# Optimization experiments

Hardware: AMD Instinct MI355X
Metric: run time of the kernel (lower is better)

## Reference

```python
import jax, jax.numpy as jnp
import numpy as np

B, N, D = 4, 2048, 1024
H = 16
DH = D // H


def setup_inputs() -> dict:
    key = jax.random.key(0)
    ks = jax.random.split(key, 9)
    s_in = 1.0 / np.sqrt(D)
    x = jax.random.normal(ks[0], (B, N, D), dtype=jnp.float32)
    Wq = jax.random.uniform(ks[1], (D, D), jnp.float32, -s_in, s_in)
    bq = jax.random.uniform(ks[2], (D,), jnp.float32, -s_in, s_in)
    Wk = jax.random.uniform(ks[3], (D, D), jnp.float32, -s_in, s_in)
    bk = jax.random.uniform(ks[4], (D,), jnp.float32, -s_in, s_in)
    Wv = jax.random.uniform(ks[5], (D, D), jnp.float32, -s_in, s_in)
    bv = jax.random.uniform(ks[6], (D,), jnp.float32, -s_in, s_in)
    Wo = jax.random.uniform(ks[7], (D, D), jnp.float32, -s_in, s_in)
    bo = jax.random.uniform(ks[8], (D,), jnp.float32, -s_in, s_in)
    return {"x": x, "Wq": Wq, "bq": bq, "Wk": Wk, "bk": bk,
            "Wv": Wv, "bv": bv, "Wo": Wo, "bo": bo}


def reference(x, Wq, bq, Wk, bk, Wv, bv, Wo, bo):
    b, n, d = x.shape
    q = (x @ Wq + bq).reshape(b, n, H, DH)  # (b, n, h, dh)
    k = (x @ Wk + bk).reshape(b, n, H, DH)
    v = (x @ Wv + bv).reshape(b, n, H, DH)
    scale = 1.0 / jnp.sqrt(jnp.asarray(DH, x.dtype))
    scores = jnp.einsum("bqhd,bkhd->bhqk", q, k) * scale  # (b, h, n, n)
    # valid = arange(1..n) per query => causal mask: key index < valid[q] = q+1
    causal = jnp.arange(n)[None, :] <= jnp.arange(n)[:, None]  # (n_q, n_k)
    scores = jnp.where(causal[None, None, :, :], scores, -jnp.inf)
    weights = jax.nn.softmax(scores, axis=-1)
    out = jnp.einsum("bhqk,bkhd->bqhd", weights, v).reshape(b, n, d)
    return out @ Wo + bo
```

## Files before the change

### kernel.cpp

```cpp
#include <hip/hip_runtime.h>
#include <hip/hip_bf16.h>
#include <math.h>

namespace {
constexpr int B_ = 4, N_ = 2048, D_ = 1024, H_ = 16, DH_ = 64;
constexpr int M_ = B_ * N_;
}

typedef __bf16 bf16x8 __attribute__((ext_vector_type(8)));
typedef __bf16 bf16x4 __attribute__((ext_vector_type(4)));
typedef float  f32x4  __attribute__((ext_vector_type(4)));

__device__ inline void async_copy16(const void* g, void* l) {
    __builtin_amdgcn_global_load_lds(
        (const __attribute__((address_space(1))) unsigned int*)g,
        (__attribute__((address_space(3))) unsigned int*)l, 16, 0, 0);
}

__device__ inline float fast_exp2(float x) {
#if __has_builtin(__builtin_amdgcn_exp2f)
    return __builtin_amdgcn_exp2f(x);
#else
    return exp2f(x);
#endif
}

__device__ inline int swz(int row, int c) {
    return c ^ (row & 3) ^ ((row >> 2) & 3);
}

__global__ __launch_bounds__(256) void cast_xw(
        const float* __restrict__ x, __bf16* __restrict__ xb,
        const float* __restrict__ Wq, const float* __restrict__ Wk,
        const float* __restrict__ Wv, const float* __restrict__ Wo,
        __bf16* __restrict__ wqkvt, __bf16* __restrict__ wot)
{
    __shared__ float t[64][65];
    const int bid = blockIdx.x;
    const int tid = threadIdx.x;
    if (bid < 4096) {
        const size_t i = ((size_t)bid * 256 + tid) * 8;
        const float4 a = *reinterpret_cast<const float4*>(x + i);
        const float4 b = *reinterpret_cast<const float4*>(x + i + 4);
        bf16x8 o;
        o[0] = (__bf16)a.x; o[1] = (__bf16)a.y; o[2] = (__bf16)a.z; o[3] = (__bf16)a.w;
        o[4] = (__bf16)b.x; o[5] = (__bf16)b.y; o[6] = (__bf16)b.z; o[7] = (__bf16)b.w;
        *reinterpret_cast<bf16x8*>(xb + i) = o;
    } else {
        const int b2 = bid - 4096;
        const int bx = b2 & 15, by = (b2 >> 4) & 15, z = b2 >> 8;
        const float* W = (z == 0) ? Wq : (z == 1) ? Wk : (z == 2) ? Wv : Wo;
        __bf16* dst = (z < 3) ? (wqkvt + (size_t)z * D_ * D_) : wot;
        const int k0 = bx * 64, n0 = by * 64;
        #pragma unroll
        for (int p = 0; p < 16; ++p) {
            const int idx = p * 256 + tid;
            const int r = idx >> 6, c = idx & 63;
            t[r][c] = W[(size_t)(k0 + r) * D_ + n0 + c];
        }
        __syncthreads();
        #pragma unroll
        for (int p = 0; p < 16; ++p) {
            const int idx = p * 256 + tid;
            const int r = idx >> 6, c = idx & 63;
            dst[(size_t)(n0 + r) * D_ + k0 + c] = (__bf16)t[c][r];
        }
    }
}

__global__ __launch_bounds__(256) void qkv_mfma(
        const __bf16* __restrict__ A, const __bf16* __restrict__ Bt,
        const float* __restrict__ bq, const float* __restrict__ bk,
        const float* __restrict__ bv,
        __bf16* __restrict__ qo, __bf16* __restrict__ ko, __bf16* __restrict__ vo)
{
    __shared__ __align__(16) __bf16 As[128 * 32];
    __shared__ __align__(16) __bf16 Bs[128 * 32];
    const int tid = threadIdx.x;
    const int w = tid >> 6, lane = tid & 63;
    const int l15 = lane & 15, quad = lane >> 4;
    const int tm = blockIdx.x * 128;
    const int tn = blockIdx.y * 128;

    f32x4 acc[4][4] = {};

    for (int k0 = 0; k0 < D_; k0 += 32) {
        __syncthreads();
        #pragma unroll
        for (int it = 0; it < 2; ++it) {
            const int c = it * 256 + tid;
            const int r = c >> 2, pc = c & 3;
            const int lc = swz(r, pc);
            async_copy16(A + (size_t)(tm + r) * D_ + k0 + lc * 8, As + c * 8);
            async_copy16(Bt + (size_t)(tn + r) * D_ + k0 + lc * 8, Bs + c * 8);
        }
        __syncthreads();

        bf16x8 af[4], bfr[4];
        #pragma unroll
        for (int t = 0; t < 4; ++t) {
            const int row = (w >> 1) * 64 + t * 16 + l15;
            af[t] = *reinterpret_cast<const bf16x8*>(
                As + (row * 4 + swz(row, quad)) * 8);
            const int col = (w & 1) * 64 + t * 16 + l15;
            bfr[t] = *reinterpret_cast<const bf16x8*>(
                Bs + (col * 4 + swz(col, quad)) * 8);
        }
        #pragma unroll
        for (int mt = 0; mt < 4; ++mt)
            #pragma unroll
            for (int nt = 0; nt < 4; ++nt)
                acc[mt][nt] = __builtin_amdgcn_mfma_f32_16x16x32_bf16(
                    af[mt], bfr[nt], acc[mt][nt], 0, 0, 0);
    }

    const int z = blockIdx.y >> 3;
    const float* bias = (z == 0) ? bq : (z == 1) ? bk : bv;
    const int col0 = (blockIdx.y & 7) * 128 + (w & 1) * 64;
    const int h = col0 >> 6;
    float bcol[4];
    #pragma unroll
    for (int nt = 0; nt < 4; ++nt) bcol[nt] = bias[col0 + nt * 16 + l15];
    const int gr0 = tm + (w >> 1) * 64;

    if (z < 2) {
        __bf16* dst = (z == 0) ? qo : ko;
        const float sc = (z == 0) ? 0.125f * 1.44269504f : 1.0f;
        #pragma unroll
        for (int mt = 0; mt < 4; ++mt)
            #pragma unroll
            for (int i = 0; i < 4; ++i) {
                const int gr = gr0 + mt * 16 + quad * 4 + i;
                const int b = gr >> 11, tok = gr & (N_ - 1);
                __bf16* row = dst + ((size_t)(b * H_ + h) * N_ + tok) * DH_;
                #pragma unroll
                for (int nt = 0; nt < 4; ++nt)
                    row[nt * 16 + l15] = (__bf16)((acc[mt][nt][i] + bcol[nt]) * sc);
            }
    } else {
        #pragma unroll
        for (int mt = 0; mt < 4; ++mt) {
            const int gr = gr0 + mt * 16 + quad * 4;
            const int b = gr >> 11, tok = gr & (N_ - 1);
            #pragma unroll
            for (int nt = 0; nt < 4; ++nt) {
                const int dh = nt * 16 + l15;
                bf16x4 pv;
                #pragma unroll
                for (int i = 0; i < 4; ++i)
                    pv[i] = (__bf16)(acc[mt][nt][i] + bcol[nt]);
                *reinterpret_cast<bf16x4*>(
                    vo + ((size_t)(b * H_ + h) * DH_ + dh) * N_ + tok) = pv;
            }
        }
    }
}

__global__ __launch_bounds__(256) void out_mfma(
        const __bf16* __restrict__ A, const __bf16* __restrict__ Bt,
        const float* __restrict__ bias, float* __restrict__ out)
{
    __shared__ __align__(16) __bf16 As[128 * 32];
    __shared__ __align__(16) __bf16 Bs[128 * 32];
    const int tid = threadIdx.x;
    const int w = tid >> 6, lane = tid & 63;
    const int l15 = lane & 15, quad = lane >> 4;
    const int tm = blockIdx.x * 128;
    const int tn = blockIdx.y * 128;

    f32x4 acc[4][4] = {};

    for (int k0 = 0; k0 < D_; k0 += 32) {
        __syncthreads();
        #pragma unroll
        for (int it = 0; it < 2; ++it) {
            const int c = it * 256 + tid;
            const int r = c >> 2, pc = c & 3;
            const int lc = swz(r, pc);
            async_copy16(A + (size_t)(tm + r) * D_ + k0 + lc * 8, As + c * 8);
            async_copy16(Bt + (size_t)(tn + r) * D_ + k0 + lc * 8, Bs + c * 8);
        }
        __syncthreads();

        bf16x8 af[4], bfr[4];
        #pragma unroll
        for (int t = 0; t < 4; ++t) {
            const int row = (w >> 1) * 64 + t * 16 + l15;
            af[t] = *reinterpret_cast<const bf16x8*>(
                As + (row * 4 + swz(row, quad)) * 8);
            const int col = (w & 1) * 64 + t * 16 + l15;
            bfr[t] = *reinterpret_cast<const bf16x8*>(
                Bs + (col * 4 + swz(col, quad)) * 8);
        }
        #pragma unroll
        for (int mt = 0; mt < 4; ++mt)
            #pragma unroll
            for (int nt = 0; nt < 4; ++nt)
                acc[mt][nt] = __builtin_amdgcn_mfma_f32_16x16x32_bf16(
                    af[mt], bfr[nt], acc[mt][nt], 0, 0, 0);
    }

    const int col0 = tn + (w & 1) * 64;
    float bcol[4];
    #pragma unroll
    for (int nt = 0; nt < 4; ++nt) bcol[nt] = bias[col0 + nt * 16 + l15];
    const int gr0 = tm + (w >> 1) * 64;
    #pragma unroll
    for (int mt = 0; mt < 4; ++mt)
        #pragma unroll
        for (int i = 0; i < 4; ++i) {
            const int gr = gr0 + mt * 16 + quad * 4 + i;
            float* row = out + (size_t)gr * D_;
            #pragma unroll
            for (int nt = 0; nt < 4; ++nt)
                row[col0 + nt * 16 + l15] = acc[mt][nt][i] + bcol[nt];
        }
}

__global__ __launch_bounds__(256, 2) void attn(
        const __bf16* __restrict__ Q, const __bf16* __restrict__ K,
        const __bf16* __restrict__ Vt, __bf16* __restrict__ ctx)
{
    const int blk = blockIdx.x;
    const int bh = blk & 63;
    const int pp = blk >> 6;
    const int tid = threadIdx.x;
    const int w = tid >> 6, lane = tid & 63;
    const int l15 = lane & 15, quad = lane >> 4;

    __shared__ __align__(16) __bf16 Ks[2][64 * 64];
    __shared__ __align__(16) __bf16 Vs[2][64 * 64];
    __shared__ __align__(16) __bf16 Ps[4][2][16 * 72];

    const __bf16* Kg = K + (size_t)bh * N_ * DH_;
    const __bf16* Vg = Vt + (size_t)bh * DH_ * N_;
    const int b = bh >> 4, h = bh & 15;
    const int sr = lane >> 3;
    const int sc = lane & 7;

    const int qbL = 15 - pp, qbS = pp;
    const int qt0L = qbL * 128, qt0S = qbS * 128;
    const int nkbL = 2 * qbL + 2, nkbS = 2 * qbS + 2;

    auto stage = [&](int kb) {
        const int sl = kb & 1;
        #pragma unroll
        for (int j = 0; j < 2; ++j) {
            const int r = j * 32 + w * 8 + sr;
            const int cl = sc ^ (r & 7);
            async_copy16(Kg + (size_t)(kb * 64 + r) * DH_ + cl * 8,
                         &Ks[sl][(j * 256 + tid) * 8]);
            async_copy16(Vg + (size_t)r * N_ + kb * 64 + cl * 8,
                         &Vs[sl][(j * 256 + tid) * 8]);
        }
    };

    bf16x8 bqfL[2][2], bqfS[2][2];
    #pragma unroll
    for (int qc = 0; qc < 2; ++qc) {
        const size_t baseL =
            ((size_t)bh * N_ + qt0L + w * 32 + qc * 16 + l15) * DH_;
        bqfL[qc][0] = *reinterpret_cast<const bf16x8*>(Q + baseL + quad * 8);
        bqfL[qc][1] = *reinterpret_cast<const bf16x8*>(Q + baseL + 32 + quad * 8);
        const size_t baseS =
            ((size_t)bh * N_ + qt0S + w * 32 + qc * 16 + l15) * DH_;
        bqfS[qc][0] = *reinterpret_cast<const bf16x8*>(Q + baseS + quad * 8);
        bqfS[qc][1] = *reinterpret_cast<const bf16x8*>(Q + baseS + 32 + quad * 8);
    }

    f32x4 accL[2][4] = {}, accS[2][4] = {};
    float llL[2] = {0.f, 0.f}, llS[2] = {0.f, 0.f};

    auto tile_qb = [&](const __bf16* Ksl, const __bf16* Vsl,
                       bf16x8 (&bqf)[2][2], f32x4 (&acc)[2][4],
                       float (&ll)[2], int qt0, int diag0, int kb) {
        f32x4 st[2][4];
        __builtin_amdgcn_s_setprio(1);
        #pragma unroll
        for (int ct = 0; ct < 4; ++ct) {
            const int row = ct * 16 + l15;
            const bf16x8 ka0 = *reinterpret_cast<const bf16x8*>(
                &Ksl[(row * 8 + (quad ^ (row & 7))) * 8]);
            const bf16x8 ka1 = *reinterpret_cast<const bf16x8*>(
                &Ksl[(row * 8 + ((quad + 4) ^ (row & 7))) * 8]);
            #pragma unroll
            for (int qc = 0; qc < 2; ++qc) {
                f32x4 t = {};
                t = __builtin_amdgcn_mfma_f32_16x16x32_bf16(ka0, bqf[qc][0], t, 0, 0, 0);
                t = __builtin_amdgcn_mfma_f32_16x16x32_bf16(ka1, bqf[qc][1], t, 0, 0, 0);
                st[qc][ct] = t;
            }
        }
        __builtin_amdgcn_s_setprio(0);
        if (kb >= diag0) {
            #pragma unroll
            for (int qc = 0; qc < 2; ++qc) {
                const int q_glob = qt0 + w * 32 + qc * 16 + l15;
                #pragma unroll
                for (int ct = 0; ct < 4; ++ct)
                    #pragma unroll
                    for (int i = 0; i < 4; ++i) {
                        const int k_glob = kb * 64 + ct * 16 + quad * 4 + i;
                        if (k_glob > q_glob) st[qc][ct][i] = -INFINITY;
                    }
            }
        }
        #pragma unroll
        for (int qc = 0; qc < 2; ++qc) {
            float rs = 0.f;
            #pragma unroll
            for (int ct = 0; ct < 4; ++ct) {
                bf16x4 pk;
                #pragma unroll
                for (int i = 0; i < 4; ++i) {
                    const float p = fast_exp2(st[qc][ct][i]);
                    rs += p;
                    pk[i] = (__bf16)p;
                }
                *reinterpret_cast<bf16x4*>(
                    &Ps[w][qc][l15 * 72 + ct * 16 + quad * 4]) = pk;
            }
            ll[qc] += rs;
        }
        bf16x8 pa0[2], pa1[2];
        #pragma unroll
        for (int qc = 0; qc < 2; ++qc) {
            pa0[qc] = *reinterpret_cast<const bf16x8*>(
                &Ps[w][qc][l15 * 72 + quad * 8]);
            pa1[qc] = *reinterpret_cast<const bf16x8*>(
                &Ps[w][qc][l15 * 72 + 32 + quad * 8]);
        }
        __builtin_amdgcn_s_setprio(1);
        #pragma unroll
        for (int ct = 0; ct < 4; ++ct) {
            const int row = ct * 16 + l15;
            const bf16x8 vb0 = *reinterpret_cast<const bf16x8*>(
                &Vsl[(row * 8 + (quad ^ (row & 7))) * 8]);
            const bf16x8 vb1 = *reinterpret_cast<const bf16x8*>(
                &Vsl[(row * 8 + ((quad + 4) ^ (row & 7))) * 8]);
            #pragma unroll
            for (int qc = 0; qc < 2; ++qc) {
                f32x4 t = acc[qc][ct];
                t = __builtin_amdgcn_mfma_f32_16x16x32_bf16(pa0[qc], vb0, t, 0, 0, 0);
                t = __builtin_amdgcn_mfma_f32_16x16x32_bf16(pa1[qc], vb1, t, 0, 0, 0);
                acc[qc][ct] = t;
            }
        }
        __builtin_amdgcn_s_setprio(0);
    };

    stage(0);
    asm volatile("s_waitcnt vmcnt(0)" ::: "memory");
    __builtin_amdgcn_s_barrier();

    #pragma unroll 1
    for (int kb = 0; kb < nkbL; ++kb) {
        const int sl = kb & 1;
        if (kb + 1 < nkbL) stage(kb + 1);
        const __bf16* Ksl = Ks[sl];
        const __bf16* Vsl = Vs[sl];

        tile_qb(Ksl, Vsl, bqfL, accL, llL, qt0L, 2 * qbL, kb);
        if (kb < nkbS)
            tile_qb(Ksl, Vsl, bqfS, accS, llS, qt0S, 2 * qbS, kb);

        asm volatile("s_waitcnt vmcnt(0)" ::: "memory");
        __builtin_amdgcn_s_barrier();
    }

    auto epilogue = [&](f32x4 (&acc)[2][4], float (&ll)[2], int qt0) {
        #pragma unroll
        for (int qc = 0; qc < 2; ++qc) {
            float r = ll[qc];
            r += __shfl_xor(r, 16);
            r += __shfl_xor(r, 32);
            const float linv = 1.0f / r;
            float lT[4];
            #pragma unroll
            for (int i = 0; i < 4; ++i) lT[i] = __shfl(linv, quad * 4 + i);
            #pragma unroll
            for (int i = 0; i < 4; ++i) {
                const int row = qt0 + w * 32 + qc * 16 + quad * 4 + i;
                __bf16* dst = ctx + ((size_t)b * N_ + row) * D_ + h * DH_;
                #pragma unroll
                for (int ct = 0; ct < 4; ++ct)
                    dst[ct * 16 + l15] = (__bf16)(acc[qc][ct][i] * lT[i]);
            }
        }
    };
    epilogue(accL, llL, qt0L);
    epilogue(accS, llS, qt0S);
}

extern "C" void kernel_launch(void* const* d_in, const int* in_sizes, int n_in,
                              void* d_out, int out_size, void* d_ws, size_t ws_size,
                              hipStream_t stream) {
    const float* x  = (const float*)d_in[0];
    const float* Wq = (const float*)d_in[1];
    const float* bq = (const float*)d_in[2];
    const float* Wk = (const float*)d_in[3];
    const float* bk = (const float*)d_in[4];
    const float* Wv = (const float*)d_in[5];
    const float* bv = (const float*)d_in[6];
    const float* Wo = (const float*)d_in[7];
    const float* bo = (const float*)d_in[8];
    float* out = (float*)d_out;

    __bf16* xb    = (__bf16*)d_ws;
    __bf16* wqkvt = xb + (size_t)M_ * D_;
    __bf16* wot   = wqkvt + (size_t)3 * D_ * D_;
    __bf16* q     = wot + (size_t)D_ * D_;
    __bf16* k     = q + (size_t)M_ * D_;
    __bf16* vt    = k + (size_t)M_ * D_;
    __bf16* ctx   = vt + (size_t)M_ * D_;

    cast_xw<<<dim3(4096 + 1024), 256, 0, stream>>>(
        x, xb, Wq, Wk, Wv, Wo, wqkvt, wot);
    qkv_mfma<<<dim3(M_ / 128, 3 * D_ / 128), 256, 0, stream>>>(
        xb, wqkvt, bq, bk, bv, q, k, vt);
    attn<<<dim3(512), 256, 0, stream>>>(q, k, vt, ctx);
    out_mfma<<<dim3(M_ / 128, D_ / 128), 256, 0, stream>>>(ctx, wot, bo, out);
}
```

Measured before the change: 243.0 us.

## Load K/V fragments directly from global memory instead of LDS double-buffering

Removes the LDS double-buffered async staging of K and V tiles, along with the per-iteration waitcnt and barrier, and has each wave read its K and V MFMA fragments straight from global memory. It also interleaves the long and short query blocks in one pass so each K/V fragment loaded into registers serves both. This frees LDS and removes block-wide sync, at the cost of redundant global and L2 traffic across the four waves and exposed load latency without explicit prefetch.

Measured after the change: 301.5 us. 1.24x slower.

```diff
diff --git a/kernel.cpp b/kernel.cpp
--- a/kernel.cpp
+++ b/kernel.cpp
@@ -228,32 +228,15 @@
     const int w = tid >> 6, lane = tid & 63;
     const int l15 = lane & 15, quad = lane >> 4;
 
-    __shared__ __align__(16) __bf16 Ks[2][64 * 64];
-    __shared__ __align__(16) __bf16 Vs[2][64 * 64];
     __shared__ __align__(16) __bf16 Ps[4][2][16 * 72];
 
     const __bf16* Kg = K + (size_t)bh * N_ * DH_;
     const __bf16* Vg = Vt + (size_t)bh * DH_ * N_;
     const int b = bh >> 4, h = bh & 15;
-    const int sr = lane >> 3;
-    const int sc = lane & 7;
 
     const int qbL = 15 - pp, qbS = pp;
     const int qt0L = qbL * 128, qt0S = qbS * 128;
     const int nkbL = 2 * qbL + 2, nkbS = 2 * qbS + 2;
-
-    auto stage = [&](int kb) {
-        const int sl = kb & 1;
-        #pragma unroll
-        for (int j = 0; j < 2; ++j) {
-            const int r = j * 32 + w * 8 + sr;
-            const int cl = sc ^ (r & 7);
-            async_copy16(Kg + (size_t)(kb * 64 + r) * DH_ + cl * 8,
-                         &Ks[sl][(j * 256 + tid) * 8]);
-            async_copy16(Vg + (size_t)r * N_ + kb * 64 + cl * 8,
-                         &Vs[sl][(j * 256 + tid) * 8]);
-        }
-    };
 
     bf16x8 bqfL[2][2], bqfS[2][2];
     #pragma unroll
@@ -271,40 +254,22 @@
     f32x4 accL[2][4] = {}, accS[2][4] = {};
     float llL[2] = {0.f, 0.f}, llS[2] = {0.f, 0.f};
 
-    auto tile_qb = [&](const __bf16* Ksl, const __bf16* Vsl,
-                       bf16x8 (&bqf)[2][2], f32x4 (&acc)[2][4],
-                       float (&ll)[2], int qt0, int diag0, int kb) {
-        f32x4 st[2][4];
-        __builtin_amdgcn_s_setprio(1);
-        #pragma unroll
-        for (int ct = 0; ct < 4; ++ct) {
-            const int row = ct * 16 + l15;
-            const bf16x8 ka0 = *reinterpret_cast<const bf16x8*>(
-                &Ksl[(row * 8 + (quad ^ (row & 7))) * 8]);
-            const bf16x8 ka1 = *reinterpret_cast<const bf16x8*>(
-                &Ksl[(row * 8 + ((quad + 4) ^ (row & 7))) * 8]);
-            #pragma unroll
-            for (int qc = 0; qc < 2; ++qc) {
-                f32x4 t = {};
-                t = __builtin_amdgcn_mfma_f32_16x16x32_bf16(ka0, bqf[qc][0], t, 0, 0, 0);
-                t = __builtin_amdgcn_mfma_f32_16x16x32_bf16(ka1, bqf[qc][1], t, 0, 0, 0);
-                st[qc][ct] = t;
-            }
-        }
-        __builtin_amdgcn_s_setprio(0);
-        if (kb >= diag0) {
-            #pragma unroll
-            for (int qc = 0; qc < 2; ++qc) {
-                const int q_glob = qt0 + w * 32 + qc * 16 + l15;
-                #pragma unroll
-                for (int ct = 0; ct < 4; ++ct)
-                    #pragma unroll
-                    for (int i = 0; i < 4; ++i) {
-                        const int k_glob = kb * 64 + ct * 16 + quad * 4 + i;
-                        if (k_glob > q_glob) st[qc][ct][i] = -INFINITY;
-                    }
-            }
-        }
+    auto mask_st = [&](f32x4 (&st)[2][4], int qt0, int kb) {
+        #pragma unroll
+        for (int qc = 0; qc < 2; ++qc) {
+            const int q_glob = qt0 + w * 32 + qc * 16 + l15;
+            #pragma unroll
+            for (int ct = 0; ct < 4; ++ct)
+                #pragma unroll
+                for (int i = 0; i < 4; ++i) {
+                    const int k_glob = kb * 64 + ct * 16 + quad * 4 + i;
+                    if (k_glob > q_glob) st[qc][ct][i] = -INFINITY;
+                }
+        }
+    };
+
+    auto softmax_frags = [&](f32x4 (&st)[2][4], float (&ll)[2],
+                             bf16x8 (&pa0)[2], bf16x8 (&pa1)[2]) {
         #pragma unroll
         for (int qc = 0; qc < 2; ++qc) {
             float rs = 0.f;
@@ -322,7 +287,6 @@
             }
             ll[qc] += rs;
         }
-        bf16x8 pa0[2], pa1[2];
         #pragma unroll
         for (int qc = 0; qc < 2; ++qc) {
             pa0[qc] = *reinterpret_cast<const bf16x8*>(
@@ -330,42 +294,75 @@
             pa1[qc] = *reinterpret_cast<const bf16x8*>(
                 &Ps[w][qc][l15 * 72 + 32 + quad * 8]);
         }
+    };
+
+    #pragma unroll 1
+    for (int kb = 0; kb < nkbL; ++kb) {
+        const bool doS = (kb < nkbS);
+        const __bf16* Kt = Kg + (size_t)kb * 64 * DH_;
+        const __bf16* Vc = Vg + (size_t)kb * 64;
+
+        f32x4 stL[2][4], stS[2][4];
+        __builtin_amdgcn_s_setprio(1);
+        #pragma unroll
+        for (int ct = 0; ct < 4; ++ct) {
+            const int row = ct * 16 + l15;
+            const bf16x8 ka0 = *reinterpret_cast<const bf16x8*>(
+                Kt + (size_t)row * DH_ + quad * 8);
+            const bf16x8 ka1 = *reinterpret_cast<const bf16x8*>(
+                Kt + (size_t)row * DH_ + 32 + quad * 8);
+            #pragma unroll
+            for (int qc = 0; qc < 2; ++qc) {
+                f32x4 t = {};
+                t = __builtin_amdgcn_mfma_f32_16x16x32_bf16(ka0, bqfL[qc][0], t, 0, 0, 0);
+                t = __builtin_amdgcn_mfma_f32_16x16x32_bf16(ka1, bqfL[qc][1], t, 0, 0, 0);
+                stL[qc][ct] = t;
+            }
+            if (doS) {
+                #pragma unroll
+                for (int qc = 0; qc < 2; ++qc) {
+                    f32x4 t = {};
+                    t = __builtin_amdgcn_mfma_f32_16x16x32_bf16(ka0, bqfS[qc][0], t, 0, 0, 0);
+                    t = __builtin_amdgcn_mfma_f32_16x16x32_bf16(ka1, bqfS[qc][1], t, 0, 0, 0);
+                    stS[qc][ct] = t;
+                }
+            }
+        }
+        __builtin_amdgcn_s_setprio(0);
+
+        if (kb >= 2 * qbL) mask_st(stL, qt0L, kb);
+        if (doS && kb >= 2 * qbS) mask_st(stS, qt0S, kb);
+
+        bf16x8 paL0[2], paL1[2], paS0[2], paS1[2];
+        softmax_frags(stL, llL, paL0, paL1);
+        if (doS) softmax_frags(stS, llS, paS0, paS1);
+
         __builtin_amdgcn_s_setprio(1);
         #pragma unroll
         for (int ct = 0; ct < 4; ++ct) {
             const int row = ct * 16 + l15;
             const bf16x8 vb0 = *reinterpret_cast<const bf16x8*>(
-                &Vsl[(row * 8 + (quad ^ (row & 7))) * 8]);
+                Vc + (size_t)row * N_ + quad * 8);
             const bf16x8 vb1 = *reinterpret_cast<const bf16x8*>(
-                &Vsl[(row * 8 + ((quad + 4) ^ (row & 7))) * 8]);
+                Vc + (size_t)row * N_ + 32 + quad * 8);
             #pragma unroll
             for (int qc = 0; qc < 2; ++qc) {
-                f32x4 t = acc[qc][ct];
-                t = __builtin_amdgcn_mfma_f32_16x16x32_bf16(pa0[qc], vb0, t, 0, 0, 0);
-                t = __builtin_amdgcn_mfma_f32_16x16x32_bf16(pa1[qc], vb1, t, 0, 0, 0);
-                acc[qc][ct] = t;
+                f32x4 t = accL[qc][ct];
+                t = __builtin_amdgcn_mfma_f32_16x16x32_bf16(paL0[qc], vb0, t, 0, 0, 0);
+                t = __builtin_amdgcn_mfma_f32_16x16x32_bf16(paL1[qc], vb1, t, 0, 0, 0);
+                accL[qc][ct] = t;
+            }
+            if (doS) {
+                #pragma unroll
+                for (int qc = 0; qc < 2; ++qc) {
+                    f32x4 t = accS[qc][ct];
+                    t = __builtin_amdgcn_mfma_f32_16x16x32_bf16(paS0[qc], vb0, t, 0, 0, 0);
+                    t = __builtin_amdgcn_mfma_f32_16x16x32_bf16(paS1[qc], vb1, t, 0, 0, 0);
+                    accS[qc][ct] = t;
+                }
             }
         }
         __builtin_amdgcn_s_setprio(0);
-    };
-
-    stage(0);
-    asm volatile("s_waitcnt vmcnt(0)" ::: "memory");
-    __builtin_amdgcn_s_barrier();
-
-    #pragma unroll 1
-    for (int kb = 0; kb < nkbL; ++kb) {
-        const int sl = kb & 1;
-        if (kb + 1 < nkbL) stage(kb + 1);
-        const __bf16* Ksl = Ks[sl];
-        const __bf16* Vsl = Vs[sl];
-
-        tile_qb(Ksl, Vsl, bqfL, accL, llL, qt0L, 2 * qbL, kb);
-        if (kb < nkbS)
-            tile_qb(Ksl, Vsl, bqfS, accS, llS, qt0S, 2 * qbS, kb);
-
-        asm volatile("s_waitcnt vmcnt(0)" ::: "memory");
-        __builtin_amdgcn_s_barrier();
     }
 
     auto epilogue = [&](f32x4 (&acc)[2][4], float (&ll)[2], int qt0) {
```

## Fuse attention and output projection into one persistent kernel with grid barrier

Applied to the files above, without the earlier changes.

Merges the attention kernel and the output-projection GEMM into a single launch. After attention, all 512 blocks meet at a global atomic-counter barrier, then each block reuses its LDS to compute one 128x128 tile of the output projection. This is meant to remove one kernel launch and the gap between kernels. It depends on all 512 blocks being co-resident (2 per CU on 256 CUs), and otherwise deadlocks. It also adds a memset for the counter and a spin-wait.

Measured after the change: 310.7 us. 27.9% more time.

```diff
diff --git a/kernel.cpp b/kernel.cpp
--- a/kernel.cpp
+++ b/kernel.cpp
@@ -156,240 +156,252 @@
     }
 }
 
-__global__ __launch_bounds__(256) void out_mfma(
-        const __bf16* __restrict__ A, const __bf16* __restrict__ Bt,
-        const float* __restrict__ bias, float* __restrict__ out)
+__global__ __launch_bounds__(256, 2) void attn_out(
+        const __bf16* __restrict__ Q, const __bf16* __restrict__ K,
+        const __bf16* __restrict__ Vt, __bf16* __restrict__ ctx,
+        const __bf16* __restrict__ wot, const float* __restrict__ bo,
+        float* __restrict__ out, unsigned* __restrict__ cnt)
 {
-    __shared__ __align__(16) __bf16 As[128 * 32];
-    __shared__ __align__(16) __bf16 Bs[128 * 32];
+    __shared__ __align__(16) unsigned char lds_raw[51200];
+
+    const int blk = blockIdx.x;
     const int tid = threadIdx.x;
     const int w = tid >> 6, lane = tid & 63;
     const int l15 = lane & 15, quad = lane >> 4;
-    const int tm = blockIdx.x * 128;
-    const int tn = blockIdx.y * 128;
-
-    f32x4 acc[4][4] = {};
-
-    for (int k0 = 0; k0 < D_; k0 += 32) {
-        __syncthreads();
-        #pragma unroll
-        for (int it = 0; it < 2; ++it) {
-            const int c = it * 256 + tid;
-            const int r = c >> 2, pc = c & 3;
-            const int lc = swz(r, pc);
-            async_copy16(A + (size_t)(tm + r) * D_ + k0 + lc * 8, As + c * 8);
-            async_copy16(Bt + (size_t)(tn + r) * D_ + k0 + lc * 8, Bs + c * 8);
-        }
-        __syncthreads();
-
-        bf16x8 af[4], bfr[4];
-        #pragma unroll
-        for (int t = 0; t < 4; ++t) {
-            const int row = (w >> 1) * 64 + t * 16 + l15;
-            af[t] = *reinterpret_cast<const bf16x8*>(
-                As + (row * 4 + swz(row, quad)) * 8);
-            const int col = (w & 1) * 64 + t * 16 + l15;
-            bfr[t] = *reinterpret_cast<const bf16x8*>(
-                Bs + (col * 4 + swz(col, quad)) * 8);
-        }
-        #pragma unroll
-        for (int mt = 0; mt < 4; ++mt)
-            #pragma unroll
-            for (int nt = 0; nt < 4; ++nt)
-                acc[mt][nt] = __builtin_amdgcn_mfma_f32_16x16x32_bf16(
-                    af[mt], bfr[nt], acc[mt][nt], 0, 0, 0);
-    }
-
-    const int col0 = tn + (w & 1) * 64;
-    float bcol[4];
-    #pragma unroll
-    for (int nt = 0; nt < 4; ++nt) bcol[nt] = bias[col0 + nt * 16 + l15];
-    const int gr0 = tm + (w >> 1) * 64;
-    #pragma unroll
-    for (int mt = 0; mt < 4; ++mt)
-        #pragma unroll
-        for (int i = 0; i < 4; ++i) {
-            const int gr = gr0 + mt * 16 + quad * 4 + i;
-            float* row = out + (size_t)gr * D_;
-            #pragma unroll
-            for (int nt = 0; nt < 4; ++nt)
-                row[col0 + nt * 16 + l15] = acc[mt][nt][i] + bcol[nt];
-        }
-}
-
-__global__ __launch_bounds__(256, 2) void attn(
-        const __bf16* __restrict__ Q, const __bf16* __restrict__ K,
-        const __bf16* __restrict__ Vt, __bf16* __restrict__ ctx)
-{
-    const int blk = blockIdx.x;
-    const int bh = blk & 63;
-    const int pp = blk >> 6;
-    const int tid = threadIdx.x;
-    const int w = tid >> 6, lane = tid & 63;
-    const int l15 = lane & 15, quad = lane >> 4;
-
-    __shared__ __align__(16) __bf16 Ks[2][64 * 64];
-    __shared__ __align__(16) __bf16 Vs[2][64 * 64];
-    __shared__ __align__(16) __bf16 Ps[4][2][16 * 72];
-
-    const __bf16* Kg = K + (size_t)bh * N_ * DH_;
-    const __bf16* Vg = Vt + (size_t)bh * DH_ * N_;
-    const int b = bh >> 4, h = bh & 15;
-    const int sr = lane >> 3;
-    const int sc = lane & 7;
-
-    const int qbL = 15 - pp, qbS = pp;
-    const int qt0L = qbL * 128, qt0S = qbS * 128;
-    const int nkbL = 2 * qbL + 2, nkbS = 2 * qbS + 2;
-
-    auto stage = [&](int kb) {
-        const int sl = kb & 1;
-        #pragma unroll
-        for (int j = 0; j < 2; ++j) {
-            const int r = j * 32 + w * 8 + sr;
-            const int cl = sc ^ (r & 7);
-            async_copy16(Kg + (size_t)(kb * 64 + r) * DH_ + cl * 8,
-                         &Ks[sl][(j * 256 + tid) * 8]);
-            async_copy16(Vg + (size_t)r * N_ + kb * 64 + cl * 8,
-                         &Vs[sl][(j * 256 + tid) * 8]);
-        }
-    };
-
-    bf16x8 bqfL[2][2], bqfS[2][2];
-    #pragma unroll
-    for (int qc = 0; qc < 2; ++qc) {
-        const size_t baseL =
-            ((size_t)bh * N_ + qt0L + w * 32 + qc * 16 + l15) * DH_;
-        bqfL[qc][0] = *reinterpret_cast<const bf16x8*>(Q + baseL + quad * 8);
-        bqfL[qc][1] = *reinterpret_cast<const bf16x8*>(Q + baseL + 32 + quad * 8);
-        const size_t baseS =
-            ((size_t)bh * N_ + qt0S + w * 32 + qc * 16 + l15) * DH_;
-        bqfS[qc][0] = *reinterpret_cast<const bf16x8*>(Q + baseS + quad * 8);
-        bqfS[qc][1] = *reinterpret_cast<const bf16x8*>(Q + baseS + 32 + quad * 8);
-    }
-
-    f32x4 accL[2][4] = {}, accS[2][4] = {};
-    float llL[2] = {0.f, 0.f}, llS[2] = {0.f, 0.f};
-
-    auto tile_qb = [&](const __bf16* Ksl, const __bf16* Vsl,
-                       bf16x8 (&bqf)[2][2], f32x4 (&acc)[2][4],
-                       float (&ll)[2], int qt0, int diag0, int kb) {
-        f32x4 st[2][4];
-        __builtin_amdgcn_s_setprio(1);
-        #pragma unroll
-        for (int ct = 0; ct < 4; ++ct) {
-            const int row = ct * 16 + l15;
-            const bf16x8 ka0 = *reinterpret_cast<const bf16x8*>(
-                &Ksl[(row * 8 + (quad ^ (row & 7))) * 8]);
-            const bf16x8 ka1 = *reinterpret_cast<const bf16x8*>(
-                &Ksl[(row * 8 + ((quad + 4) ^ (row & 7))) * 8]);
+
+    {
+        __bf16 (*Ks)[64 * 64] = reinterpret_cast<__bf16(*)[64 * 64]>(lds_raw);
+        __bf16 (*Vs)[64 * 64] =
+            reinterpret_cast<__bf16(*)[64 * 64]>(lds_raw + 16384);
+        __bf16* Psb = reinterpret_cast<__bf16*>(lds_raw + 32768);
+        auto PsAt = [&](int qc) { return Psb + (w * 2 + qc) * (16 * 72); };
+
+        const int bh = blk & 63;
+        const int pp = blk >> 6;
+        const __bf16* Kg = K + (size_t)bh * N_ * DH_;
+        const __bf16* Vg = Vt + (size_t)bh * DH_ * N_;
+        const int b = bh >> 4, h = bh & 15;
+        const int sr = lane >> 3;
+        const int sc = lane & 7;
+
+        const int qbL = 15 - pp, qbS = pp;
+        const int qt0L = qbL * 128, qt0S = qbS * 128;
+        const int nkbL = 2 * qbL + 2, nkbS = 2 * qbS + 2;
+
+        auto stage = [&](int kb) {
+            const int sl = kb & 1;
+            #pragma unroll
+            for (int j = 0; j < 2; ++j) {
+                const int r = j * 32 + w * 8 + sr;
+                const int cl = sc ^ (r & 7);
+                async_copy16(Kg + (size_t)(kb * 64 + r) * DH_ + cl * 8,
+                             &Ks[sl][(j * 256 + tid) * 8]);
+                async_copy16(Vg + (size_t)r * N_ + kb * 64 + cl * 8,
+                             &Vs[sl][(j * 256 + tid) * 8]);
+            }
+        };
+
+        bf16x8 bqfL[2][2], bqfS[2][2];
+        #pragma unroll
+        for (int qc = 0; qc < 2; ++qc) {
+            const size_t baseL =
+                ((size_t)bh * N_ + qt0L + w * 32 + qc * 16 + l15) * DH_;
+            bqfL[qc][0] = *reinterpret_cast<const bf16x8*>(Q + baseL + quad * 8);
+            bqfL[qc][1] = *reinterpret_cast<const bf16x8*>(Q + baseL + 32 + quad * 8);
+            const size_t baseS =
+                ((size_t)bh * N_ + qt0S + w * 32 + qc * 16 + l15) * DH_;
+            bqfS[qc][0] = *reinterpret_cast<const bf16x8*>(Q + baseS + quad * 8);
+            bqfS[qc][1] = *reinterpret_cast<const bf16x8*>(Q + baseS + 32 + quad * 8);
+        }
+
+        f32x4 accL[2][4] = {}, accS[2][4] = {};
+        float llL[2] = {0.f, 0.f}, llS[2] = {0.f, 0.f};
+
+        auto tile_qb = [&](const __bf16* Ksl, const __bf16* Vsl,
+                           bf16x8 (&bqf)[2][2], f32x4 (&acc)[2][4],
+                           float (&ll)[2], int qt0, int diag0, int kb) {
+            f32x4 st[2][4];
+            __builtin_amdgcn_s_setprio(1);
+            #pragma unroll
+            for (int ct = 0; ct < 4; ++ct) {
+                const int row = ct * 16 + l15;
+                const bf16x8 ka0 = *reinterpret_cast<const bf16x8*>(
+                    &Ksl[(row * 8 + (quad ^ (row & 7))) * 8]);
+                const bf16x8 ka1 = *reinterpret_cast<const bf16x8*>(
+                    &Ksl[(row * 8 + ((quad + 4) ^ (row & 7))) * 8]);
+                #pragma unroll
+                for (int qc = 0; qc < 2; ++qc) {
+                    f32x4 t = {};
+                    t = __builtin_amdgcn_mfma_f32_16x16x32_bf16(ka0, bqf[qc][0], t, 0, 0, 0);
+                    t = __builtin_amdgcn_mfma_f32_16x16x32_bf16(ka1, bqf[qc][1], t, 0, 0, 0);
+                    st[qc][ct] = t;
+                }
+            }
+            __builtin_amdgcn_s_setprio(0);
+            if (kb >= diag0) {
+                #pragma unroll
+                for (int qc = 0; qc < 2; ++qc) {
+                    const int q_glob = qt0 + w * 32 + qc * 16 + l15;
+                    #pragma unroll
+                    for (int ct = 0; ct < 4; ++ct)
+                        #pragma unroll
+                        for (int i = 0; i < 4; ++i) {
+                            const int k_glob = kb * 64 + ct * 16 + quad * 4 + i;
+                            if (k_glob > q_glob) st[qc][ct][i] = -INFINITY;
+                        }
+                }
+            }
             #pragma unroll
             for (int qc = 0; qc < 2; ++qc) {
-                f32x4 t = {};
-                t = __builtin_amdgcn_mfma_f32_16x16x32_bf16(ka0, bqf[qc][0], t, 0, 0, 0);
-                t = __builtin_amdgcn_mfma_f32_16x16x32_bf16(ka1, bqf[qc][1], t, 0, 0, 0);
-                st[qc][ct] = t;
-            }
-        }
-        __builtin_amdgcn_s_setprio(0);
-        if (kb >= diag0) {
-            #pragma unroll
-            for (int qc = 0; qc < 2; ++qc) {
-                const int q_glob = qt0 + w * 32 + qc * 16 + l15;
-                #pragma unroll
-                for (int ct = 0; ct < 4; ++ct)
+                float rs = 0.f;
+                #pragma unroll
+                for (int ct = 0; ct < 4; ++ct) {
+                    bf16x4 pk;
                     #pragma unroll
                     for (int i = 0; i < 4; ++i) {
-                        const int k_glob = kb * 64 + ct * 16 + quad * 4 + i;
-                        if (k_glob > q_glob) st[qc][ct][i] = -INFINITY;
+                        const float p = fast_exp2(st[qc][ct][i]);
+                        rs += p;
+                        pk[i] = (__bf16)p;
                     }
-            }
-        }
-        #pragma unroll
-        for (int qc = 0; qc < 2; ++qc) {
-            float rs = 0.f;
+                    *reinterpret_cast<bf16x4*>(
+                        &PsAt(qc)[l15 * 72 + ct * 16 + quad * 4]) = pk;
+                }
+                ll[qc] += rs;
+            }
+            bf16x8 pa0[2], pa1[2];
+            #pragma unroll
+            for (int qc = 0; qc < 2; ++qc) {
+                pa0[qc] = *reinterpret_cast<const bf16x8*>(
+                    &PsAt(qc)[l15 * 72 + quad * 8]);
+                pa1[qc] = *reinterpret_cast<const bf16x8*>(
+                    &PsAt(qc)[l15 * 72 + 32 + quad * 8]);
+            }
+            __builtin_amdgcn_s_setprio(1);
             #pragma unroll
             for (int ct = 0; ct < 4; ++ct) {
-                bf16x4 pk;
-                #pragma unroll
-                for (int i = 0; i < 4; ++i) {
-                    const float p = fast_exp2(st[qc][ct][i]);
-                    rs += p;
-                    pk[i] = (__bf16)p;
+                const int row = ct * 16 + l15;
+                const bf16x8 vb0 = *reinterpret_cast<const bf16x8*>(
+                    &Vsl[(row * 8 + (quad ^ (row & 7))) * 8]);
+                const bf16x8 vb1 = *reinterpret_cast<const bf16x8*>(
+                    &Vsl[(row * 8 + ((quad + 4) ^ (row & 7))) * 8]);
+                #pragma unroll
+                for (int qc = 0; qc < 2; ++qc) {
+                    f32x4 t = acc[qc][ct];
+                    t = __builtin_amdgcn_mfma_f32_16x16x32_bf16(pa0[qc], vb0, t, 0, 0, 0);
+                    t = __builtin_amdgcn_mfma_f32_16x16x32_bf16(pa1[qc], vb1, t, 0, 0, 0);
+                    acc[qc][ct] = t;
                 }
-                *reinterpret_cast<bf16x4*>(
-                    &Ps[w][qc][l15 * 72 + ct * 16 + quad * 4]) = pk;
-            }
-            ll[qc] += rs;
-        }
-        bf16x8 pa0[2], pa1[2];
-        #pragma unroll
-        for (int qc = 0; qc < 2; ++qc) {
-            pa0[qc] = *reinterpret_cast<const bf16x8*>(
-                &Ps[w][qc][l15 * 72 + quad * 8]);
-            pa1[qc] = *reinterpret_cast<const bf16x8*>(
-                &Ps[w][qc][l15 * 72 + 32 + quad * 8]);
-        }
-        __builtin_amdgcn_s_setprio(1);
-        #pragma unroll
-        for (int ct = 0; ct < 4; ++ct) {
-            const int row = ct * 16 + l15;
-            const bf16x8 vb0 = *reinterpret_cast<const bf16x8*>(
-                &Vsl[(row * 8 + (quad ^ (row & 7))) * 8]);
-            const bf16x8 vb1 = *reinterpret_cast<const bf16x8*>(
-                &Vsl[(row * 8 + ((quad + 4) ^ (row & 7))) * 8]);
-            #pragma unroll
-            for (int qc = 0; qc < 2; ++qc) {
-                f32x4 t = acc[qc][ct];
-                t = __builtin_amdgcn_mfma_f32_16x16x32_bf16(pa0[qc], vb0, t, 0, 0, 0);
-                t = __builtin_amdgcn_mfma_f32_16x16x32_bf16(pa1[qc], vb1, t, 0, 0, 0);
-                acc[qc][ct] = t;
-            }
-        }
-        __builtin_amdgcn_s_setprio(0);
-    };
-
-    stage(0);
-    asm volatile("s_waitcnt vmcnt(0)" ::: "memory");
-    __builtin_amdgcn_s_barrier();
-
-    #pragma unroll 1
-    for (int kb = 0; kb < nkbL; ++kb) {
-        const int sl = kb & 1;
-        if (kb + 1 < nkbL) stage(kb + 1);
-        const __bf16* Ksl = Ks[sl];
-        const __bf16* Vsl = Vs[sl];
-
-        tile_qb(Ksl, Vsl, bqfL, accL, llL, qt0L, 2 * qbL, kb);
-        if (kb < nkbS)
-            tile_qb(Ksl, Vsl, bqfS, accS, llS, qt0S, 2 * qbS, kb);
-
+            }
+            __builtin_amdgcn_s_setprio(0);
+        };
+
+        stage(0);
         asm volatile("s_waitcnt vmcnt(0)" ::: "memory");
         __builtin_amdgcn_s_barrier();
-    }
-
-    auto epilogue = [&](f32x4 (&acc)[2][4], float (&ll)[2], int qt0) {
-        #pragma unroll
-        for (int qc = 0; qc < 2; ++qc) {
-            float r = ll[qc];
-            r += __shfl_xor(r, 16);
-            r += __shfl_xor(r, 32);
-            const float linv = 1.0f / r;
-            float lT[4];
-            #pragma unroll
-            for (int i = 0; i < 4; ++i) lT[i] = __shfl(linv, quad * 4 + i);
+
+        #pragma unroll 1
+        for (int kb = 0; kb < nkbL; ++kb) {
+            const int sl = kb & 1;
+            if (kb + 1 < nkbL) stage(kb + 1);
+            const __bf16* Ksl = Ks[sl];
+            const __bf16* Vsl = Vs[sl];
+
+            tile_qb(Ksl, Vsl, bqfL, accL, llL, qt0L, 2 * qbL, kb);
+            if (kb < nkbS)
+                tile_qb(Ksl, Vsl, bqfS, accS, llS, qt0S, 2 * qbS, kb);
+
+            asm volatile("s_waitcnt vmcnt(0)" ::: "memory");
+            __builtin_amdgcn_s_barrier();
+        }
+
+        auto epilogue = [&](f32x4 (&acc)[2][4], float (&ll)[2], int qt0) {
+            #pragma unroll
+            for (int qc = 0; qc < 2; ++qc) {
+                float r = ll[qc];
+                r += __shfl_xor(r, 16);
+                r += __shfl_xor(r, 32);
+                const float linv = 1.0f / r;
+                float lT[4];
+                #pragma unroll
+                for (int i = 0; i < 4; ++i) lT[i] = __shfl(linv, quad * 4 + i);
+                #pragma unroll
+                for (int i = 0; i < 4; ++i) {
+                    const int row = qt0 + w * 32 + qc * 16 + quad * 4 + i;
+                    __bf16* dst = ctx + ((size_t)b * N_ + row) * D_ + h * DH_;
+                    #pragma unroll
+                    for (int ct = 0; ct < 4; ++ct)
+                        dst[ct * 16 + l15] = (__bf16)(acc[qc][ct][i] * lT[i]);
+                }
+            }
+        };
+        epilogue(accL, llL, qt0L);
+        epilogue(accS, llS, qt0S);
+    }
+
+    __syncthreads();
+    if (tid == 0) {
+        __hip_atomic_fetch_add(cnt, 1u, __ATOMIC_RELEASE,
+                               __HIP_MEMORY_SCOPE_AGENT);
+        while (__hip_atomic_load(cnt, __ATOMIC_ACQUIRE,
+                                 __HIP_MEMORY_SCOPE_AGENT) < 512u)
+            __builtin_amdgcn_s_sleep(8);
+    }
+    __syncthreads();
+
+    {
+        __bf16* As = reinterpret_cast<__bf16*>(lds_raw);
+        __bf16* Bs = As + 128 * 32;
+        const int tm = (blk & 63) * 128;
+        const int tn = (blk >> 6) * 128;
+
+        f32x4 acc[4][4] = {};
+
+        for (int k0 = 0; k0 < D_; k0 += 32) {
+            __syncthreads();
+            #pragma unroll
+            for (int it = 0; it < 2; ++it) {
+                const int c = it * 256 + tid;
+                const int r = c >> 2, pc = c & 3;
+                const int lc = swz(r, pc);
+                async_copy16(ctx + (size_t)(tm + r) * D_ + k0 + lc * 8, As + c * 8);
+                async_copy16(wot + (size_t)(tn + r) * D_ + k0 + lc * 8, Bs + c * 8);
+            }
+            __syncthreads();
+
+            bf16x8 af[4], bfr[4];
+            #pragma unroll
+            for (int t = 0; t < 4; ++t) {
+                const int row = (w >> 1) * 64 + t * 16 + l15;
+                af[t] = *reinterpret_cast<const bf16x8*>(
+                    As + (row * 4 + swz(row, quad)) * 8);
+                const int col = (w & 1) * 64 + t * 16 + l15;
+                bfr[t] = *reinterpret_cast<const bf16x8*>(
+                    Bs + (col * 4 + swz(col, quad)) * 8);
+            }
+            #pragma unroll
+            for (int mt = 0; mt < 4; ++mt)
+                #pragma unroll
+                for (int nt = 0; nt < 4; ++nt)
+                    acc[mt][nt] = __builtin_amdgcn_mfma_f32_16x16x32_bf16(
+                        af[mt], bfr[nt], acc[mt][nt], 0, 0, 0);
+        }
+
+        const int col0 = tn + (w & 1) * 64;
+        float bcol[4];
+        #pragma unroll
+        for (int nt = 0; nt < 4; ++nt) bcol[nt] = bo[col0 + nt * 16 + l15];
+        const int gr0 = tm + (w >> 1) * 64;
+        #pragma unroll
+        for (int mt = 0; mt < 4; ++mt)
             #pragma unroll
             for (int i = 0; i < 4; ++i) {
-                const int row = qt0 + w * 32 + qc * 16 + quad * 4 + i;
-                __bf16* dst = ctx + ((size_t)b * N_ + row) * D_ + h * DH_;
-                #pragma unroll
-                for (int ct = 0; ct < 4; ++ct)
-                    dst[ct * 16 + l15] = (__bf16)(acc[qc][ct][i] * lT[i]);
-            }
-        }
-    };
-    epilogue(accL, llL, qt0L);
-    epilogue(accS, llS, qt0S);
+                const int gr = gr0 + mt * 16 + quad * 4 + i;
+                float* row = out + (size_t)gr * D_;
+                #pragma unroll
+                for (int nt = 0; nt < 4; ++nt)
+                    row[col0 + nt * 16 + l15] = acc[mt][nt][i] + bcol[nt];
+            }
+    }
 }
 
 extern "C" void kernel_launch(void* const* d_in, const int* in_sizes, int n_in,
@@ -413,11 +425,12 @@
     __bf16* k     = q + (size_t)M_ * D_;
     __bf16* vt    = k + (size_t)M_ * D_;
     __bf16* ctx   = vt + (size_t)M_ * D_;
-
+    unsigned* cnt = (unsigned*)(ctx + (size_t)M_ * D_);
+
+    hipMemsetAsync(cnt, 0, sizeof(unsigned), stream);
     cast_xw<<<dim3(4096 + 1024), 256, 0, stream>>>(
         x, xb, Wq, Wk, Wv, Wo, wqkvt, wot);
     qkv_mfma<<<dim3(M_ / 128, 3 * D_ / 128), 256, 0, stream>>>(
         xb, wqkvt, bq, bk, bv, q, k, vt);
-    attn<<<dim3(512), 256, 0, stream>>>(q, k, vt, ctx);
-    out_mfma<<<dim3(M_ / 128, D_ / 128), 256, 0, stream>>>(ctx, wot, bo, out);
-}
+    attn_out<<<dim3(512), 256, 0, stream>>>(q, k, vt, ctx, wot, bo, out, cnt);
+}
```
